# Optimization experiments

Hardware: AMD Instinct MI355X
Metric: run time of the kernel (lower is better)

Reference implementation:

```python
import jax, jax.numpy as jnp
import numpy as np

N_REL = 16   # n_relation
EMB = 512    # emb_size
N = 32768    # number of nodes/tokens


def setup_inputs() -> dict:
    key = jax.random.key(0)
    k1, k2, k3 = jax.random.split(key, 3)
    node_emb = jax.random.normal(k1, (N, EMB), dtype=jnp.float32)
    relation = jax.random.randint(k2, (N,), 0, N_REL)
    # nn.Linear default init: U(-1/sqrt(in_features), 1/sqrt(in_features))
    bound = 1.0 / np.sqrt(EMB)
    W = jax.random.uniform(k3, (N_REL, EMB, EMB), dtype=jnp.float32,
                           minval=-bound, maxval=bound)
    return {"node_emb": node_emb, "relation": relation, "W": W}


def reference(node_emb, relation, W):
    # out[i] = W[relation[i]] @ node_emb[i]  (F.linear(x, W_r) == x @ W_r.T)
    # Loop over the small fixed relation set via lax.scan; tokens stay vectorized.
    n_rel = W.shape[0]
    out0 = jnp.zeros((node_emb.shape[0], W.shape[1]), dtype=node_emb.dtype)

    def body(acc, wr):
        Wr, r = wr
        y = node_emb @ Wr.T                       # [N, EMB]
        acc = jnp.where((relation == r)[:, None], y, acc)
        return acc, None

    out, _ = jax.lax.scan(body, out0, (W, jnp.arange(n_rel)))
    return out
```

## Files before the change

### kernel.cpp

```cpp
#include <hip/hip_runtime.h>
#include <stdint.h>


#define EMB 512
#define N_RELC 16
#define BM 128
#define BN 256
#define BK 32
#define NKT 16

typedef __attribute__((ext_vector_type(4))) float f32x4;
typedef __attribute__((ext_vector_type(8))) short bf16x8;

__device__ __forceinline__ unsigned short f2bf(float f) {
  unsigned int u = __float_as_uint(f);
  u += 0x7FFFu + ((u >> 16) & 1u);
  return (unsigned short)(u >> 16);
}

__device__ __forceinline__ bf16x8 cvt8(f32x4 lo, f32x4 hi) {
  bf16x8 o;
  o[0] = (short)f2bf(lo[0]); o[1] = (short)f2bf(lo[1]);
  o[2] = (short)f2bf(lo[2]); o[3] = (short)f2bf(lo[3]);
  o[4] = (short)f2bf(hi[0]); o[5] = (short)f2bf(hi[1]);
  o[6] = (short)f2bf(hi[2]); o[7] = (short)f2bf(hi[3]);
  return o;
}

__device__ __forceinline__ void gload_lds16(const void* g, void* l) {
  __builtin_amdgcn_global_load_lds(
      (const __attribute__((address_space(1))) unsigned int*)(uintptr_t)g,
      (__attribute__((address_space(3))) unsigned int*)(uintptr_t)l, 16, 0, 0);
}

__global__ void init_counts(int* cnt) {
  if (threadIdx.x < 32) cnt[threadIdx.x] = 0;
}

__global__ __launch_bounds__(256) void histo_rank_fill(
    const int* __restrict__ rel, int* cnt, int* pos, int* ptok,
    int n, int padn) {
  __shared__ int lcnt[N_RELC];
  __shared__ int lbase[N_RELC];
  const int tid = threadIdx.x;
  if (tid < N_RELC) lcnt[tid] = 0;
  __syncthreads();
  const int i = blockIdx.x * blockDim.x + tid;
  if (i < padn) ptok[i] = -1;
  int r = 0, myrank = 0;
  if (i < n) { r = rel[i]; myrank = atomicAdd(&lcnt[r], 1); }
  __syncthreads();
  if (tid < N_RELC) lbase[tid] = atomicAdd(&cnt[tid], lcnt[tid]);
  __syncthreads();
  if (i < n) pos[i] = lbase[r] + myrank;
}

__global__ void prefix_tiles64(const int* __restrict__ cnt, int* pbase,
                               int* tinfo, int maxt) {
  __shared__ int sb[N_RELC + 1];
  __shared__ int st[N_RELC + 1];
  if (threadIdx.x == 0) {
    int acc = 0, t = 0;
    for (int r = 0; r < N_RELC; ++r) {
      sb[r] = acc; st[r] = t;
      const int nt = (cnt[r] + BM - 1) / BM;
      acc += nt * BM;
      t += nt;
    }
    sb[N_RELC] = acc; st[N_RELC] = t;
  }
  __syncthreads();
  for (int i = threadIdx.x; i <= N_RELC; i += blockDim.x) pbase[i] = sb[i];
  for (int x = threadIdx.x; x < maxt; x += blockDim.x) {
    int v = -1;
    #pragma unroll
    for (int r = 0; r < N_RELC; ++r)
      if (x >= st[r] && x < st[r + 1]) v = (r << 16) | (x - st[r]);
    tinfo[x] = v;
  }
}

__global__ __launch_bounds__(256) void scatter_ptok(
    const int* __restrict__ rel, const int* __restrict__ pos,
    const int* __restrict__ pbase, int* __restrict__ ptok, int n) {
  const int i = blockIdx.x * blockDim.x + threadIdx.x;
  if (i < n) ptok[pbase[rel[i]] + pos[i]] = i;
}

__global__ __launch_bounds__(256) void convert_W(const float* __restrict__ W,
                                                 unsigned short* __restrict__ Ws,
                                                 int welems) {
  const size_t i = ((size_t)blockIdx.x * 256 + threadIdx.x) * 8;
  if (i >= (size_t)welems) return;
  f32x4 a = *reinterpret_cast<const f32x4*>(W + i);
  f32x4 c = *reinterpret_cast<const f32x4*>(W + i + 4);
  bf16x8 o;
  o[0] = f2bf(a[0]); o[1] = f2bf(a[1]); o[2] = f2bf(a[2]); o[3] = f2bf(a[3]);
  o[4] = f2bf(c[0]); o[5] = f2bf(c[1]); o[6] = f2bf(c[2]); o[7] = f2bf(c[3]);
  *reinterpret_cast<bf16x8*>(Ws + i) = o;
}


#define ALOAD(P, KT)                                                           \
  {                                                                            \
    const float* ap_ = aptr + (KT) * BK;                                       \
    a##P##0 = *reinterpret_cast<const f32x4*>(ap_);                            \
    a##P##1 = *reinterpret_cast<const f32x4*>(ap_ + 4);                        \
  }

#define AWRITE(S, P)                                                           \
  {                                                                            \
    bf16x8 w_ = cvt8(a##P##0, a##P##1);                                        \
    *reinterpret_cast<bf16x8*>((char*)&As[S][0] + awoff) = w_;                 \
  }

#define BSTAGE(S, KT)                                                          \
  {                                                                            \
    const int kb_ = (KT) * BK;                                                 \
    gload_lds16(bsrc0 + kb_, (char*)&Bs[S][0] + tid * 16);                     \
    gload_lds16(bsrc1 + kb_, (char*)&Bs[S][0] + 8192 + tid * 16);              \
  }

#define COMPUTE(S)                                                             \
  {                                                                            \
    bf16x8 af[4], bfr[4];                                                      \
    _Pragma("unroll")                                                          \
    for (int m = 0; m < 4; ++m) {                                              \
      const int rr_ = wr * 64 + m * 16 + lrow;                                 \
      af[m] = *reinterpret_cast<const bf16x8*>(                                \
          (const char*)&As[S][0] + rr_ * 64 + ((gl ^ ((rr_ >> 1) & 3)) * 16)); \
    }                                                                          \
    _Pragma("unroll")                                                          \
    for (int nn = 0; nn < 4; ++nn) {                                           \
      const int rw_ = wc * 64 + nn * 16 + lrow;                                \
      bfr[nn] = *reinterpret_cast<const bf16x8*>(                              \
          (const char*)&Bs[S][0] + rw_ * 64 + ((gl ^ ((rw_ >> 1) & 3)) * 16)); \
    }                                                                          \
    __builtin_amdgcn_s_setprio(1);                                             \
    _Pragma("unroll")                                                          \
    for (int m = 0; m < 4; ++m)                                                \
      _Pragma("unroll")                                                        \
      for (int nn = 0; nn < 4; ++nn)                                           \
        acc[m][nn] = __builtin_amdgcn_mfma_f32_16x16x32_bf16(                  \
            af[m], bfr[nn], acc[m][nn], 0, 0, 0);                              \
    __builtin_amdgcn_s_setprio(0);                                             \
  }

#define ITER(T, VM)                                                            \
  {                                                                            \
    if ((T) + 2 < NKT) {                                                       \
      if (((T) & 1) == 0) ALOAD(e, (T) + 2) else ALOAD(o, (T) + 2)             \
      __builtin_amdgcn_sched_barrier(0);                                       \
      BSTAGE(((T) + 2) % 3, (T) + 2);                                          \
      __builtin_amdgcn_sched_barrier(0);                                       \
    }                                                                          \
    asm volatile("s_waitcnt vmcnt(" #VM ")" ::: "memory");                     \
    __builtin_amdgcn_s_barrier();                                              \
    __builtin_amdgcn_sched_barrier(0);                                         \
    if ((T) + 1 < NKT) {                                                       \
      if ((((T) + 1) & 1) == 0) AWRITE(((T) + 1) % 3, e)                       \
      else                      AWRITE(((T) + 1) % 3, o)                       \
    }                                                                          \
    COMPUTE((T) % 3);                                                          \
    asm volatile("s_waitcnt lgkmcnt(0)" ::: "memory");                         \
    __builtin_amdgcn_s_barrier();                                              \
    __builtin_amdgcn_sched_barrier(0);                                         \
  }

__global__ __launch_bounds__(512, 4) void gg13(
    const float* __restrict__ X, const unsigned short* __restrict__ Ws,
    const int* __restrict__ pbase, const int* __restrict__ tinfo,
    const int* __restrict__ ptok, float* __restrict__ out)
{
  __shared__ unsigned short As[3][BM * BK];
  __shared__ unsigned short Bs[3][BN * BK];

  const int q = gridDim.x >> 3;
  const int lid = ((int)blockIdx.x & 7) * q + ((int)blockIdx.x >> 3);
  const int info = tinfo[lid >> 1];
  if (info < 0) return;
  const int r = info >> 16;
  const int mt = info & 0xFFFF;
  const int ct = lid & 1;
  const int prow0 = pbase[r] + mt * BM;

  const int tid = threadIdx.x;
  const int lane = tid & 63;
  const int wid = tid >> 6;
  const int wr = wid >> 2;
  const int wc = wid & 3;
  const int lrow = lane & 15;
  const int gl = lane >> 4;

  const int srow = tid >> 2;
  const int lg = tid & 3;
  const int awoff = srow * 64 + ((lg ^ ((srow >> 1) & 3)) * 16);
  int tokA = ptok[prow0 + srow];
  if (tokA < 0) tokA = 0;
  const float* aptr = X + (size_t)tokA * EMB + lg * 8;

  const int blg = (tid & 3) ^ ((tid >> 3) & 3);
  const unsigned short* bsrc0 =
      Ws + ((size_t)r * EMB + (size_t)(ct * BN + srow)) * EMB + blg * 8;
  const unsigned short* bsrc1 = bsrc0 + (size_t)128 * EMB;

  f32x4 acc[4][4];
  const f32x4 vzero = {0.f, 0.f, 0.f, 0.f};
  #pragma unroll
  for (int m = 0; m < 4; ++m)
    #pragma unroll
    for (int nn = 0; nn < 4; ++nn) acc[m][nn] = vzero;

  f32x4 ae0, ae1, ao0, ao1;

  ALOAD(e, 0)
  __builtin_amdgcn_sched_barrier(0);
  BSTAGE(0, 0);
  __builtin_amdgcn_sched_barrier(0);
  ALOAD(o, 1)
  __builtin_amdgcn_sched_barrier(0);
  BSTAGE(1, 1);
  __builtin_amdgcn_sched_barrier(0);
  AWRITE(0, e)

  ITER(0, 8)   ITER(1, 8)   ITER(2, 8)   ITER(3, 8)
  ITER(4, 8)   ITER(5, 8)   ITER(6, 8)   ITER(7, 8)
  ITER(8, 8)   ITER(9, 8)   ITER(10, 8)  ITER(11, 8)
  ITER(12, 8)  ITER(13, 8)  ITER(14, 4)  ITER(15, 0)

  #pragma unroll
  for (int m = 0; m < 4; ++m) {
    const int base = prow0 + wr * 64 + m * 16 + gl * 4;
    #pragma unroll
    for (int rg = 0; rg < 4; ++rg) {
      const int tok = ptok[base + rg];
      if (tok >= 0) {
        float* orow = out + (size_t)tok * EMB + ct * BN + wc * 64;
        #pragma unroll
        for (int nn = 0; nn < 4; ++nn)
          orow[nn * 16 + lrow] = acc[m][nn][rg];
      }
    }
  }
}

__global__ void naive_kernel(const float* __restrict__ X, const int* __restrict__ rel,
                             const float* __restrict__ W, float* __restrict__ out, int n) {
  int i = blockIdx.x;
  if (i >= n) return;
  int r = rel[i];
  const float* x = X + (size_t)i * EMB;
  const float* Wr = W + (size_t)r * EMB * EMB;
  for (int j = threadIdx.x; j < EMB; j += blockDim.x) {
    const float* w = Wr + (size_t)j * EMB;
    float s = 0.f;
    for (int k = 0; k < EMB; ++k) s += w[k] * x[k];
    out[(size_t)i * EMB + j] = s;
  }
}

extern "C" void kernel_launch(void* const* d_in, const int* in_sizes, int n_in,
                              void* d_out, int out_size, void* d_ws, size_t ws_size,
                              hipStream_t stream) {
  const float* X  = (const float*)d_in[0];
  const int* rel  = (const int*)d_in[1];
  const float* W  = (const float*)d_in[2];
  float* out      = (float*)d_out;
  const int n = in_sizes[1];
  const int welems = in_sizes[2];
  const int padn = n + N_RELC * BM;
  const int maxt = (n + BM - 1) / BM + N_RELC;
  const int maxtp = ((maxt + 3) / 4) * 4;

  const size_t ints = (size_t)64 + n + padn + maxtp;
  const size_t offW = ((ints * sizeof(int) + 255) / 256) * 256;
  const size_t need = offW + (size_t)welems * 2;

  if (ws_size < need) {
    naive_kernel<<<n, 256, 0, stream>>>(X, rel, W, out, n);
    return;
  }

  int* cnt   = (int*)d_ws;
  int* pbase = cnt + 16;
  int* pos   = cnt + 64;
  int* ptok  = pos + n;
  int* tinfo = ptok + padn;
  unsigned short* Ws = (unsigned short*)((char*)d_ws + offW);

  init_counts<<<1, 32, 0, stream>>>(cnt);
  histo_rank_fill<<<(padn + 255) / 256, 256, 0, stream>>>(rel, cnt, pos, ptok, n, padn);
  prefix_tiles64<<<1, 64, 0, stream>>>(cnt, pbase, tinfo, maxtp);
  scatter_ptok<<<(n + 255) / 256, 256, 0, stream>>>(rel, pos, pbase, ptok, n);
  convert_W<<<(welems / 8 + 255) / 256, 256, 0, stream>>>(W, Ws, welems);

  gg13<<<2 * maxtp, 512, 0, stream>>>(X, Ws, pbase, tinfo, ptok, out);
}
```

Before: 65.40 us.

## Drop W bf16 pre-conversion; stage fp32 W in LDS and convert on read

Removes the separate convert_W kernel and its workspace, so the grouped GEMM loads fp32 weights straight into LDS with swizzled direct-to-LDS copies and converts them to bf16 while building MFMA fragments. The tile shape drops from 128x256 with 512 threads to 128x128 with 256 threads, giving four column tiles per row tile. This removes one launch and the extra pass that reads and writes W, at the cost of twice the B traffic into LDS per tile, extra conversion ALU work inside the inner loop, and more LDS per block.

```diff
diff --git a/kernel.cpp b/kernel.cpp
--- a/kernel.cpp
+++ b/kernel.cpp
@@ -5,7 +5,7 @@
 #define EMB 512
 #define N_RELC 16
 #define BM 128
-#define BN 256
+#define BN 128
 #define BK 32
 #define NKT 16
 
@@ -87,38 +87,31 @@
   if (i < n) ptok[pbase[rel[i]] + pos[i]] = i;
 }
 
-__global__ __launch_bounds__(256) void convert_W(const float* __restrict__ W,
-                                                 unsigned short* __restrict__ Ws,
-                                                 int welems) {
-  const size_t i = ((size_t)blockIdx.x * 256 + threadIdx.x) * 8;
-  if (i >= (size_t)welems) return;
-  f32x4 a = *reinterpret_cast<const f32x4*>(W + i);
-  f32x4 c = *reinterpret_cast<const f32x4*>(W + i + 4);
-  bf16x8 o;
-  o[0] = f2bf(a[0]); o[1] = f2bf(a[1]); o[2] = f2bf(a[2]); o[3] = f2bf(a[3]);
-  o[4] = f2bf(c[0]); o[5] = f2bf(c[1]); o[6] = f2bf(c[2]); o[7] = f2bf(c[3]);
-  *reinterpret_cast<bf16x8*>(Ws + i) = o;
-}
-
 
 #define ALOAD(P, KT)                                                           \
   {                                                                            \
     const float* ap_ = aptr + (KT) * BK;                                       \
     a##P##0 = *reinterpret_cast<const f32x4*>(ap_);                            \
     a##P##1 = *reinterpret_cast<const f32x4*>(ap_ + 4);                        \
+    a##P##2 = *reinterpret_cast<const f32x4*>(ap_ + 8);                        \
+    a##P##3 = *reinterpret_cast<const f32x4*>(ap_ + 12);                       \
   }
 
 #define AWRITE(S, P)                                                           \
   {                                                                            \
-    bf16x8 w_ = cvt8(a##P##0, a##P##1);                                        \
-    *reinterpret_cast<bf16x8*>((char*)&As[S][0] + awoff) = w_;                 \
+    bf16x8 w0_ = cvt8(a##P##0, a##P##1);                                       \
+    bf16x8 w1_ = cvt8(a##P##2, a##P##3);                                       \
+    *reinterpret_cast<bf16x8*>((char*)&As[S][0] + awoff0) = w0_;               \
+    *reinterpret_cast<bf16x8*>((char*)&As[S][0] + awoff1) = w1_;               \
   }
 
 #define BSTAGE(S, KT)                                                          \
   {                                                                            \
     const int kb_ = (KT) * BK;                                                 \
     gload_lds16(bsrc0 + kb_, (char*)&Bs[S][0] + tid * 16);                     \
-    gload_lds16(bsrc1 + kb_, (char*)&Bs[S][0] + 8192 + tid * 16);              \
+    gload_lds16(bsrc1 + kb_, (char*)&Bs[S][0] + 4096 + tid * 16);              \
+    gload_lds16(bsrc2 + kb_, (char*)&Bs[S][0] + 8192 + tid * 16);              \
+    gload_lds16(bsrc3 + kb_, (char*)&Bs[S][0] + 12288 + tid * 16);             \
   }
 
 #define COMPUTE(S)                                                             \
@@ -133,8 +126,12 @@
     _Pragma("unroll")                                                          \
     for (int nn = 0; nn < 4; ++nn) {                                           \
       const int rw_ = wc * 64 + nn * 16 + lrow;                                \
-      bfr[nn] = *reinterpret_cast<const bf16x8*>(                              \
-          (const char*)&Bs[S][0] + rw_ * 64 + ((gl ^ ((rw_ >> 1) & 3)) * 16)); \
+      const char* bb_ = (const char*)&Bs[S][0] + rw_ * 128;                    \
+      f32x4 lo = *reinterpret_cast<const f32x4*>(                              \
+          bb_ + (((gl * 2) ^ (rw_ & 7)) * 16));                                \
+      f32x4 hi = *reinterpret_cast<const f32x4*>(                              \
+          bb_ + (((gl * 2 + 1) ^ (rw_ & 7)) * 16));                            \
+      bfr[nn] = cvt8(lo, hi);                                                  \
     }                                                                          \
     __builtin_amdgcn_s_setprio(1);                                             \
     _Pragma("unroll")                                                          \
@@ -167,42 +164,46 @@
     __builtin_amdgcn_sched_barrier(0);                                         \
   }
 
-__global__ __launch_bounds__(512, 4) void gg13(
-    const float* __restrict__ X, const unsigned short* __restrict__ Ws,
+__global__ __launch_bounds__(256, 2) void gg17(
+    const float* __restrict__ X, const float* __restrict__ W,
     const int* __restrict__ pbase, const int* __restrict__ tinfo,
     const int* __restrict__ ptok, float* __restrict__ out)
 {
   __shared__ unsigned short As[3][BM * BK];
-  __shared__ unsigned short Bs[3][BN * BK];
+  __shared__ float Bs[3][BN * BK];
 
   const int q = gridDim.x >> 3;
   const int lid = ((int)blockIdx.x & 7) * q + ((int)blockIdx.x >> 3);
-  const int info = tinfo[lid >> 1];
+  const int info = tinfo[lid >> 2];
   if (info < 0) return;
   const int r = info >> 16;
   const int mt = info & 0xFFFF;
-  const int ct = lid & 1;
+  const int ct = lid & 3;
   const int prow0 = pbase[r] + mt * BM;
 
   const int tid = threadIdx.x;
   const int lane = tid & 63;
   const int wid = tid >> 6;
-  const int wr = wid >> 2;
-  const int wc = wid & 3;
+  const int wr = wid >> 1, wc = wid & 1;
   const int lrow = lane & 15;
   const int gl = lane >> 4;
 
-  const int srow = tid >> 2;
-  const int lg = tid & 3;
-  const int awoff = srow * 64 + ((lg ^ ((srow >> 1) & 3)) * 16);
-  int tokA = ptok[prow0 + srow];
+  const int arow = tid >> 1;
+  const int g0 = (tid & 1) * 2;
+  const int asw = (arow >> 1) & 3;
+  const int awoff0 = arow * 64 + ((g0 ^ asw) * 16);
+  const int awoff1 = arow * 64 + (((g0 + 1) ^ asw) * 16);
+  int tokA = ptok[prow0 + arow];
   if (tokA < 0) tokA = 0;
-  const float* aptr = X + (size_t)tokA * EMB + lg * 8;
-
-  const int blg = (tid & 3) ^ ((tid >> 3) & 3);
-  const unsigned short* bsrc0 =
-      Ws + ((size_t)r * EMB + (size_t)(ct * BN + srow)) * EMB + blg * 8;
-  const unsigned short* bsrc1 = bsrc0 + (size_t)128 * EMB;
+  const float* aptr = X + (size_t)tokA * EMB + g0 * 8;
+
+  const int brow = tid >> 3;
+  const int bcol = ((tid & 7) ^ (brow & 7)) * 4;
+  const float* Wr = W + (size_t)r * EMB * EMB + (size_t)ct * BN * EMB;
+  const float* bsrc0 = Wr + (size_t)(brow)       * EMB + bcol;
+  const float* bsrc1 = Wr + (size_t)(brow + 32)  * EMB + bcol;
+  const float* bsrc2 = Wr + (size_t)(brow + 64)  * EMB + bcol;
+  const float* bsrc3 = Wr + (size_t)(brow + 96)  * EMB + bcol;
 
   f32x4 acc[4][4];
   const f32x4 vzero = {0.f, 0.f, 0.f, 0.f};
@@ -211,7 +212,7 @@
     #pragma unroll
     for (int nn = 0; nn < 4; ++nn) acc[m][nn] = vzero;
 
-  f32x4 ae0, ae1, ao0, ao1;
+  f32x4 ae0, ae1, ae2, ae3, ao0, ao1, ao2, ao3;
 
   ALOAD(e, 0)
   __builtin_amdgcn_sched_barrier(0);
@@ -222,11 +223,13 @@
   BSTAGE(1, 1);
   __builtin_amdgcn_sched_barrier(0);
   AWRITE(0, e)
-
-  ITER(0, 8)   ITER(1, 8)   ITER(2, 8)   ITER(3, 8)
-  ITER(4, 8)   ITER(5, 8)   ITER(6, 8)   ITER(7, 8)
-  ITER(8, 8)   ITER(9, 8)   ITER(10, 8)  ITER(11, 8)
-  ITER(12, 8)  ITER(13, 8)  ITER(14, 4)  ITER(15, 0)
+  asm volatile("s_waitcnt lgkmcnt(0)" ::: "memory");
+  __builtin_amdgcn_sched_barrier(0);
+
+  ITER(0, 16)  ITER(1, 16)  ITER(2, 16)  ITER(3, 16)
+  ITER(4, 16)  ITER(5, 16)  ITER(6, 16)  ITER(7, 16)
+  ITER(8, 16)  ITER(9, 16)  ITER(10, 16) ITER(11, 16)
+  ITER(12, 16) ITER(13, 16) ITER(14, 8)  ITER(15, 0)
 
   #pragma unroll
   for (int m = 0; m < 4; ++m) {
@@ -267,14 +270,11 @@
   const float* W  = (const float*)d_in[2];
   float* out      = (float*)d_out;
   const int n = in_sizes[1];
-  const int welems = in_sizes[2];
   const int padn = n + N_RELC * BM;
   const int maxt = (n + BM - 1) / BM + N_RELC;
-  const int maxtp = ((maxt + 3) / 4) * 4;
-
-  const size_t ints = (size_t)64 + n + padn + maxtp;
-  const size_t offW = ((ints * sizeof(int) + 255) / 256) * 256;
-  const size_t need = offW + (size_t)welems * 2;
+  const int maxtp = ((maxt + 1) / 2) * 2;
+
+  const size_t need = (size_t)(64 + 32 + n + padn + maxtp) * sizeof(int);
 
   if (ws_size < need) {
     naive_kernel<<<n, 256, 0, stream>>>(X, rel, W, out, n);
@@ -282,17 +282,15 @@
   }
 
   int* cnt   = (int*)d_ws;
-  int* pbase = cnt + 16;
-  int* pos   = cnt + 64;
+  int* pbase = cnt + 64;
+  int* pos   = pbase + 32;
   int* ptok  = pos + n;
   int* tinfo = ptok + padn;
-  unsigned short* Ws = (unsigned short*)((char*)d_ws + offW);
 
   init_counts<<<1, 32, 0, stream>>>(cnt);
   histo_rank_fill<<<(padn + 255) / 256, 256, 0, stream>>>(rel, cnt, pos, ptok, n, padn);
   prefix_tiles64<<<1, 64, 0, stream>>>(cnt, pbase, tinfo, maxtp);
   scatter_ptok<<<(n + 255) / 256, 256, 0, stream>>>(rel, pos, pbase, ptok, n);
-  convert_W<<<(welems / 8 + 255) / 256, 256, 0, stream>>>(W, Ws, welems);
-
-  gg13<<<2 * maxtp, 512, 0, stream>>>(X, Ws, pbase, tinfo, ptok, out);
-}
+
+  gg17<<<4 * maxtp, 256, 0, stream>>>(X, W, pbase, tinfo, ptok, out);
+}
```

Result: slower. 82.61 us (+26.3%).

## Merge preprocessing kernels and replace global atomics with per-block count prefix

Applied to the files above, without the earlier changes.

The six-launch preprocessing chain becomes four launches. The histogram/rank pass and the W-to-bf16 conversion now run as one kernel split by block index. The global atomic counter and its init kernel are replaced with per-block relation counts written to workspace, which a single-block prefix kernel turns into per-block bases for the scatter. This removes launch gaps and global atomics, but the prefix kernel now serially loops over all histogram blocks per relation (about 128 blocks here).

```diff
diff --git a/kernel.cpp b/kernel.cpp
--- a/kernel.cpp
+++ b/kernel.cpp
@@ -33,45 +33,69 @@
       (__attribute__((address_space(3))) unsigned int*)(uintptr_t)l, 16, 0, 0);
 }
 
-__global__ void init_counts(int* cnt) {
-  if (threadIdx.x < 32) cnt[threadIdx.x] = 0;
-}
-
-__global__ __launch_bounds__(256) void histo_rank_fill(
-    const int* __restrict__ rel, int* cnt, int* pos, int* ptok,
-    int n, int padn) {
-  __shared__ int lcnt[N_RELC];
-  __shared__ int lbase[N_RELC];
+__global__ __launch_bounds__(256) void prep1(
+    const int* __restrict__ rel, const float* __restrict__ W,
+    int* __restrict__ blockcnt, int* __restrict__ pos, int* __restrict__ ptok,
+    unsigned short* __restrict__ Ws,
+    int n, int padn, int nbh, int welems, int gpad)
+{
+  const int b = blockIdx.x;
   const int tid = threadIdx.x;
-  if (tid < N_RELC) lcnt[tid] = 0;
-  __syncthreads();
-  const int i = blockIdx.x * blockDim.x + tid;
-  if (i < padn) ptok[i] = -1;
-  int r = 0, myrank = 0;
-  if (i < n) { r = rel[i]; myrank = atomicAdd(&lcnt[r], 1); }
-  __syncthreads();
-  if (tid < N_RELC) lbase[tid] = atomicAdd(&cnt[tid], lcnt[tid]);
-  __syncthreads();
-  if (i < n) pos[i] = lbase[r] + myrank;
-}
-
-__global__ void prefix_tiles64(const int* __restrict__ cnt, int* pbase,
-                               int* tinfo, int maxt) {
+  if (b < gpad) {
+    __shared__ int lcnt[N_RELC];
+    if (tid < N_RELC) lcnt[tid] = 0;
+    __syncthreads();
+    const int i = b * 256 + tid;
+    if (i < padn) ptok[i] = -1;
+    if (i < n) pos[i] = atomicAdd(&lcnt[rel[i]], 1);
+    __syncthreads();
+    if (b < nbh && tid < N_RELC) blockcnt[b * N_RELC + tid] = lcnt[tid];
+  } else {
+    const size_t i = (((size_t)(b - gpad)) * 256 + tid) * 8;
+    if (i >= (size_t)welems) return;
+    f32x4 a = *reinterpret_cast<const f32x4*>(W + i);
+    f32x4 c = *reinterpret_cast<const f32x4*>(W + i + 4);
+    bf16x8 o;
+    o[0] = f2bf(a[0]); o[1] = f2bf(a[1]); o[2] = f2bf(a[2]); o[3] = f2bf(a[3]);
+    o[4] = f2bf(c[0]); o[5] = f2bf(c[1]); o[6] = f2bf(c[2]); o[7] = f2bf(c[3]);
+    *reinterpret_cast<bf16x8*>(Ws + i) = o;
+  }
+}
+
+__global__ __launch_bounds__(64) void prefix2(
+    const int* __restrict__ blockcnt, int* __restrict__ pbase,
+    int* __restrict__ bbase, int* __restrict__ tinfo, int nbh, int maxt) {
+  __shared__ int sc[N_RELC];
   __shared__ int sb[N_RELC + 1];
   __shared__ int st[N_RELC + 1];
-  if (threadIdx.x == 0) {
+  const int tid = threadIdx.x;
+  if (tid < N_RELC) {
+    int s = 0;
+    for (int b = 0; b < nbh; ++b) s += blockcnt[b * N_RELC + tid];
+    sc[tid] = s;
+  }
+  __syncthreads();
+  if (tid == 0) {
     int acc = 0, t = 0;
     for (int r = 0; r < N_RELC; ++r) {
       sb[r] = acc; st[r] = t;
-      const int nt = (cnt[r] + BM - 1) / BM;
+      const int nt = (sc[r] + BM - 1) / BM;
       acc += nt * BM;
       t += nt;
     }
     sb[N_RELC] = acc; st[N_RELC] = t;
   }
   __syncthreads();
-  for (int i = threadIdx.x; i <= N_RELC; i += blockDim.x) pbase[i] = sb[i];
-  for (int x = threadIdx.x; x < maxt; x += blockDim.x) {
+  if (tid < N_RELC) {
+    int run = sb[tid];
+    for (int b = 0; b < nbh; ++b) {
+      bbase[b * N_RELC + tid] = run;
+      run += blockcnt[b * N_RELC + tid];
+    }
+    pbase[tid] = sb[tid];
+  }
+  if (tid == 0) pbase[N_RELC] = sb[N_RELC];
+  for (int x = tid; x < maxt; x += 64) {
     int v = -1;
     #pragma unroll
     for (int r = 0; r < N_RELC; ++r)
@@ -80,24 +104,11 @@
   }
 }
 
-__global__ __launch_bounds__(256) void scatter_ptok(
+__global__ __launch_bounds__(256) void scatter2(
     const int* __restrict__ rel, const int* __restrict__ pos,
-    const int* __restrict__ pbase, int* __restrict__ ptok, int n) {
+    const int* __restrict__ bbase, int* __restrict__ ptok, int n) {
   const int i = blockIdx.x * blockDim.x + threadIdx.x;
-  if (i < n) ptok[pbase[rel[i]] + pos[i]] = i;
-}
-
-__global__ __launch_bounds__(256) void convert_W(const float* __restrict__ W,
-                                                 unsigned short* __restrict__ Ws,
-                                                 int welems) {
-  const size_t i = ((size_t)blockIdx.x * 256 + threadIdx.x) * 8;
-  if (i >= (size_t)welems) return;
-  f32x4 a = *reinterpret_cast<const f32x4*>(W + i);
-  f32x4 c = *reinterpret_cast<const f32x4*>(W + i + 4);
-  bf16x8 o;
-  o[0] = f2bf(a[0]); o[1] = f2bf(a[1]); o[2] = f2bf(a[2]); o[3] = f2bf(a[3]);
-  o[4] = f2bf(c[0]); o[5] = f2bf(c[1]); o[6] = f2bf(c[2]); o[7] = f2bf(c[3]);
-  *reinterpret_cast<bf16x8*>(Ws + i) = o;
+  if (i < n) ptok[bbase[(i >> 8) * N_RELC + rel[i]] + pos[i]] = i;
 }
 
 
@@ -167,7 +178,7 @@
     __builtin_amdgcn_sched_barrier(0);                                         \
   }
 
-__global__ __launch_bounds__(512, 4) void gg13(
+__global__ __launch_bounds__(512, 4) void gg18(
     const float* __restrict__ X, const unsigned short* __restrict__ Ws,
     const int* __restrict__ pbase, const int* __restrict__ tinfo,
     const int* __restrict__ ptok, float* __restrict__ out)
@@ -269,10 +280,12 @@
   const int n = in_sizes[1];
   const int welems = in_sizes[2];
   const int padn = n + N_RELC * BM;
+  const int nbh = (n + 255) / 256;
+  const int gpad = (padn + 255) / 256;
   const int maxt = (n + BM - 1) / BM + N_RELC;
   const int maxtp = ((maxt + 3) / 4) * 4;
 
-  const size_t ints = (size_t)64 + n + padn + maxtp;
+  const size_t ints = (size_t)32 + n + padn + maxtp + 2 * (size_t)nbh * N_RELC;
   const size_t offW = ((ints * sizeof(int) + 255) / 256) * 256;
   const size_t need = offW + (size_t)welems * 2;
 
@@ -281,18 +294,20 @@
     return;
   }
 
-  int* cnt   = (int*)d_ws;
-  int* pbase = cnt + 16;
-  int* pos   = cnt + 64;
-  int* ptok  = pos + n;
-  int* tinfo = ptok + padn;
+  int* pbase    = (int*)d_ws;
+  int* pos      = pbase + 32;
+  int* ptok     = pos + n;
+  int* tinfo    = ptok + padn;
+  int* blockcnt = tinfo + maxtp;
+  int* bbase    = blockcnt + (size_t)nbh * N_RELC;
   unsigned short* Ws = (unsigned short*)((char*)d_ws + offW);
 
-  init_counts<<<1, 32, 0, stream>>>(cnt);
-  histo_rank_fill<<<(padn + 255) / 256, 256, 0, stream>>>(rel, cnt, pos, ptok, n, padn);
-  prefix_tiles64<<<1, 64, 0, stream>>>(cnt, pbase, tinfo, maxtp);
-  scatter_ptok<<<(n + 255) / 256, 256, 0, stream>>>(rel, pos, pbase, ptok, n);
-  convert_W<<<(welems / 8 + 255) / 256, 256, 0, stream>>>(W, Ws, welems);
-
-  gg13<<<2 * maxtp, 512, 0, stream>>>(X, Ws, pbase, tinfo, ptok, out);
-}
+  const int wb = (welems / 8 + 255) / 256;
+
+  prep1<<<gpad + wb, 256, 0, stream>>>(rel, W, blockcnt, pos, ptok, Ws,
+                                       n, padn, nbh, welems, gpad);
+  prefix2<<<1, 64, 0, stream>>>(blockcnt, pbase, bbase, tinfo, nbh, maxtp);
+  scatter2<<<(n + 255) / 256, 256, 0, stream>>>(rel, pos, bbase, ptok, n);
+
+  gg18<<<2 * maxtp, 512, 0, stream>>>(X, Ws, pbase, tinfo, ptok, out);
+}
```

Result: slower. 83.77 us (+28.1%).
